# Optimization experiments

Measured on AMD Instinct MI355X. Metric: run time of the kernel, lower is better.

## Reference

```python
import jax, jax.numpy as jnp
import numpy as np

B, F, O = 4096, 16384, 256
MANTISSA_BITS = 23  # flip only mantissa bits to keep values finite


def setup_inputs() -> dict:
    key = jax.random.key(0)
    k1, k2, k3, k4 = jax.random.split(key, 4)
    x = jax.random.normal(k1, (B, F), dtype=jnp.float32)
    W = jax.random.normal(k2, (F, O), dtype=jnp.float32) * 0.02
    b = jnp.zeros((O,), dtype=jnp.float32)
    bitswap_coeff = jnp.ones((), dtype=jnp.float32)  # scalar 'bitswap_coeff' weight
    # uniform categorical over flattened features == uniform randint
    idx = jax.random.randint(k3, (B,), 0, F, dtype=jnp.int32)
    bit_positions = jax.random.randint(k4, (B,), 0, MANTISSA_BITS, dtype=jnp.int32)
    return {"x": x, "W": W, "b": b, "bitswap_coeff": bitswap_coeff,
            "idx": idx, "bit_positions": bit_positions}


def _bit_flip(g, bit_positions):
    # SimulateSwap: flip one mantissa bit of the float32 representation
    gi = jax.lax.bitcast_convert_type(g, jnp.int32)
    gi = gi ^ (jnp.int32(1) << bit_positions)
    return jax.lax.bitcast_convert_type(gi, jnp.float32)


def reference(x, W, b, bitswap_coeff, idx, bit_positions):
    rows = jnp.arange(x.shape[0])
    # gather_nd(batch_dims=1): one element per batch row
    g = x[rows, idx]                              # [B]
    updates = _bit_flip(g, bit_positions) - g     # swap_sim(x) - x
    # tensor_scatter_nd_update onto zeros, scaled by bitswap coefficient
    pert = jnp.zeros_like(x).at[rows, idx].set(updates) * bitswap_coeff
    # wrapped layer: Dense
    return (x + pert) @ W + b
```

## Files before the change

kernel.cpp:

```cpp
#include <hip/hip_runtime.h>

#define M_DIM 4096
#define K_DIM 16384
#define N_DIM 256
#define SPLIT 16

typedef __bf16 bf16x8 __attribute__((ext_vector_type(8)));
typedef __bf16 bf16x4 __attribute__((ext_vector_type(4)));
typedef float f32x4 __attribute__((ext_vector_type(4)));
typedef unsigned short us4 __attribute__((ext_vector_type(4)));

__device__ __forceinline__ unsigned short f2bf(float f) {
  unsigned int u = __float_as_uint(f);
  u += 0x7fffu + ((u >> 16) & 1u);
  return (unsigned short)(u >> 16);
}

__global__ __launch_bounds__(256) void wt_kernel(const float* __restrict__ W,
                                                 __bf16* __restrict__ Wt) {
  __shared__ float tile[64][65];
  const int k0 = blockIdx.x * 64, n0 = blockIdx.y * 64;
  const int t = threadIdx.x;
#pragma unroll
  for (int r = 0; r < 4; ++r) {
    int idx4 = r * 256 + t;
    int kr = idx4 >> 4, c4 = idx4 & 15;
    f32x4 v = *(const f32x4*)(W + (size_t)(k0 + kr) * N_DIM + n0 + c4 * 4);
#pragma unroll
    for (int j = 0; j < 4; ++j) tile[kr][c4 * 4 + j] = v[j];
  }
  __syncthreads();
#pragma unroll
  for (int r = 0; r < 4; ++r) {
    int nr = (t >> 4) + r * 16, k4 = t & 15;
    bf16x4 o;
#pragma unroll
    for (int j = 0; j < 4; ++j) o[j] = (__bf16)tile[k4 * 4 + j][nr];
    *(bf16x4*)(Wt + (size_t)(n0 + nr) * K_DIM + k0 + k4 * 4) = o;
  }
}

__global__ __launch_bounds__(256, 3) void gemm_kernel(const float* __restrict__ x,
                                                      const __bf16* __restrict__ Wt,
                                                      __bf16* __restrict__ part,
                                                      int kslice) {
  __shared__ __bf16 As[64 * 72];
  __shared__ __bf16 Bs[256 * 64];

  const int t = threadIdx.x;
  const int l = t & 63;
  const int w = t >> 6;
  const int la = l & 15, q = l >> 4;
  const int m0 = blockIdx.x * 64;
  const int kbase = blockIdx.y * kslice;

  f32x4 acc[4][4];
  const f32x4 zero = {0.f, 0.f, 0.f, 0.f};
#pragma unroll
  for (int i = 0; i < 4; ++i)
#pragma unroll
    for (int j = 0; j < 4; ++j) acc[i][j] = zero;

  const int niter = kslice >> 6;
  for (int it = 0; it < niter; ++it) {
    const int k0 = kbase + it * 64;

#pragma unroll
    for (int c = 0; c < 8; ++c) {
      int nb = w * 64 + c * 8;
      const __bf16* g = Wt + (size_t)(nb + (l & 7)) * K_DIM + k0 + ((l >> 3) * 8);
      __bf16* lp = &Bs[nb * 64];
      __builtin_amdgcn_global_load_lds((const __attribute__((address_space(1))) void*)g,
                                       (__attribute__((address_space(3))) void*)lp, 16, 0, 0);
    }

#pragma unroll
    for (int r = 0; r < 4; ++r) {
      int idx4 = r * 256 + t;
      int row = idx4 >> 4, c4 = idx4 & 15;
      f32x4 v = *(const f32x4*)(x + (size_t)(m0 + row) * K_DIM + k0 + c4 * 4);
      bf16x4 o = {(__bf16)v[0], (__bf16)v[1], (__bf16)v[2], (__bf16)v[3]};
      *(bf16x4*)(&As[row * 72 + c4 * 4]) = o;
    }
    __syncthreads();

#pragma unroll
    for (int ks = 0; ks < 2; ++ks) {
      const int kb = ks * 32 + q * 8;
      bf16x8 a[4], b[4];
#pragma unroll
      for (int i = 0; i < 4; ++i)
        a[i] = *(const bf16x8*)(&As[(i * 16 + la) * 72 + kb]);
#pragma unroll
      for (int j = 0; j < 4; ++j) {
        int n = w * 64 + j * 16 + la;
        b[j] = *(const bf16x8*)(&Bs[(n >> 3) * 512 + (kb >> 3) * 64 + (n & 7) * 8]);
      }
#pragma unroll
      for (int i = 0; i < 4; ++i)
#pragma unroll
        for (int j = 0; j < 4; ++j)
          acc[i][j] = __builtin_amdgcn_mfma_f32_16x16x32_bf16(a[i], b[j], acc[i][j], 0, 0, 0);
    }
    __syncthreads();
  }

  __bf16* pbase = part + (size_t)blockIdx.y * ((size_t)M_DIM * N_DIM);
#pragma unroll
  for (int i = 0; i < 4; ++i) {
    int r0 = m0 + i * 16 + q * 4;
#pragma unroll
    for (int j = 0; j < 4; ++j) {
      int c = w * 64 + j * 16 + la;
#pragma unroll
      for (int r = 0; r < 4; ++r)
        pbase[(size_t)(r0 + r) * N_DIM + c] = (__bf16)acc[i][j][r];
    }
  }
}

__global__ __launch_bounds__(256) void reduce_kernel(const __bf16* __restrict__ part,
                                                     const float* __restrict__ x,
                                                     const float* __restrict__ W,
                                                     const float* __restrict__ bvec,
                                                     const float* __restrict__ coeffp,
                                                     const int* __restrict__ idx,
                                                     const int* __restrict__ bp,
                                                     float* __restrict__ out) {
  const int row = blockIdx.x;
  const int o = threadIdx.x;
  const int iv = idx[row];
  const float g = x[(size_t)row * K_DIM + iv];
  const int bits = __float_as_int(g) ^ (1 << bp[row]);
  const float upd = __int_as_float(bits) - g;
  const float coeff = coeffp[0];
  const size_t off = (size_t)row * N_DIM + o;
  float sum = 0.f;
#pragma unroll
  for (int s = 0; s < SPLIT; ++s)
    sum += (float)part[(size_t)s * ((size_t)M_DIM * N_DIM) + off];
  out[off] = sum + coeff * upd * W[(size_t)iv * N_DIM + o] + bvec[o];
}

extern "C" void kernel_launch(void* const* d_in, const int* in_sizes, int n_in,
                              void* d_out, int out_size, void* d_ws, size_t ws_size,
                              hipStream_t stream) {
  const float* x = (const float*)d_in[0];
  const float* W = (const float*)d_in[1];
  const float* b = (const float*)d_in[2];
  const float* coeff = (const float*)d_in[3];
  const int* idx = (const int*)d_in[4];
  const int* bp = (const int*)d_in[5];
  float* out = (float*)d_out;

  __bf16* Wt = (__bf16*)d_ws;
  const size_t wt_bytes = (size_t)K_DIM * N_DIM * 2;
  __bf16* part = (__bf16*)((char*)d_ws + wt_bytes);

  hipLaunchKernelGGL(wt_kernel, dim3(K_DIM / 64, N_DIM / 64), dim3(256), 0, stream, W, Wt);
  hipLaunchKernelGGL(gemm_kernel, dim3(M_DIM / 64, SPLIT), dim3(256), 0, stream,
                     x, Wt, part, K_DIM / SPLIT);
  hipLaunchKernelGGL(reduce_kernel, dim3(M_DIM), dim3(256), 0, stream,
                     part, x, W, b, coeff, idx, bp, out);
}
```

Before: 435.4 us.

## Register-prefetch next K tile in GEMM, pad B smem layout, halve split-K

Replaces the direct global-to-LDS loads for the B operand with register staging, and prefetches the next iteration's A and B tiles into registers while the MFMAs run on the current tile. B shared memory becomes a padded row-major layout, and split-K drops from 16 to 8, which halves partial-sum traffic and the reduce work. The costs are higher register pressure under the 3-blocks-per-CU launch bound and half as many blocks in the GEMM grid.

```diff
diff --git a/kernel.cpp b/kernel.cpp
--- a/kernel.cpp
+++ b/kernel.cpp
@@ -3,18 +3,14 @@
 #define M_DIM 4096
 #define K_DIM 16384
 #define N_DIM 256
-#define SPLIT 16
+#define SPLIT 8
+#define BK 64
+#define KSLICE (K_DIM / SPLIT)
+#define NITER (KSLICE / BK)
 
 typedef __bf16 bf16x8 __attribute__((ext_vector_type(8)));
 typedef __bf16 bf16x4 __attribute__((ext_vector_type(4)));
 typedef float f32x4 __attribute__((ext_vector_type(4)));
-typedef unsigned short us4 __attribute__((ext_vector_type(4)));
-
-__device__ __forceinline__ unsigned short f2bf(float f) {
-  unsigned int u = __float_as_uint(f);
-  u += 0x7fffu + ((u >> 16) & 1u);
-  return (unsigned short)(u >> 16);
-}
 
 __global__ __launch_bounds__(256) void wt_kernel(const float* __restrict__ W,
                                                  __bf16* __restrict__ Wt) {
@@ -42,17 +38,30 @@
 
 __global__ __launch_bounds__(256, 3) void gemm_kernel(const float* __restrict__ x,
                                                       const __bf16* __restrict__ Wt,
-                                                      __bf16* __restrict__ part,
-                                                      int kslice) {
+                                                      __bf16* __restrict__ part) {
   __shared__ __bf16 As[64 * 72];
-  __shared__ __bf16 Bs[256 * 64];
+  __shared__ __bf16 Bs[256 * 72];
 
   const int t = threadIdx.x;
   const int l = t & 63;
   const int w = t >> 6;
   const int la = l & 15, q = l >> 4;
   const int m0 = blockIdx.x * 64;
-  const int kbase = blockIdx.y * kslice;
+  const int kbase = blockIdx.y * KSLICE;
+
+  const int arow = t >> 4, ac4 = t & 15;
+  const int bn = t >> 3, bk8 = (t & 7) * 8;
+
+  const float* ap = x + (size_t)(m0 + arow) * K_DIM + kbase + ac4 * 4;
+  const __bf16* bp = Wt + (size_t)bn * K_DIM + kbase + bk8;
+
+  f32x4 areg[4];
+  bf16x8 breg[8];
+
+#pragma unroll
+  for (int r = 0; r < 4; ++r) areg[r] = *(const f32x4*)(ap + (size_t)r * 16 * K_DIM);
+#pragma unroll
+  for (int c = 0; c < 8; ++c) breg[c] = *(const bf16x8*)(bp + (size_t)c * 32 * K_DIM);
 
   f32x4 acc[4][4];
   const f32x4 zero = {0.f, 0.f, 0.f, 0.f};
@@ -61,28 +70,27 @@
 #pragma unroll
     for (int j = 0; j < 4; ++j) acc[i][j] = zero;
 
-  const int niter = kslice >> 6;
-  for (int it = 0; it < niter; ++it) {
-    const int k0 = kbase + it * 64;
-
-#pragma unroll
-    for (int c = 0; c < 8; ++c) {
-      int nb = w * 64 + c * 8;
-      const __bf16* g = Wt + (size_t)(nb + (l & 7)) * K_DIM + k0 + ((l >> 3) * 8);
-      __bf16* lp = &Bs[nb * 64];
-      __builtin_amdgcn_global_load_lds((const __attribute__((address_space(1))) void*)g,
-                                       (__attribute__((address_space(3))) void*)lp, 16, 0, 0);
-    }
-
+  for (int it = 0; it < NITER; ++it) {
+    __syncthreads();
 #pragma unroll
     for (int r = 0; r < 4; ++r) {
-      int idx4 = r * 256 + t;
-      int row = idx4 >> 4, c4 = idx4 & 15;
-      f32x4 v = *(const f32x4*)(x + (size_t)(m0 + row) * K_DIM + k0 + c4 * 4);
-      bf16x4 o = {(__bf16)v[0], (__bf16)v[1], (__bf16)v[2], (__bf16)v[3]};
-      *(bf16x4*)(&As[row * 72 + c4 * 4]) = o;
+      bf16x4 o = {(__bf16)areg[r][0], (__bf16)areg[r][1],
+                  (__bf16)areg[r][2], (__bf16)areg[r][3]};
+      *(bf16x4*)(&As[(arow + r * 16) * 72 + ac4 * 4]) = o;
     }
+#pragma unroll
+    for (int c = 0; c < 8; ++c)
+      *(bf16x8*)(&Bs[(bn + c * 32) * 72 + bk8]) = breg[c];
     __syncthreads();
+
+    if (it + 1 < NITER) {
+      ap += BK;
+      bp += BK;
+#pragma unroll
+      for (int r = 0; r < 4; ++r) areg[r] = *(const f32x4*)(ap + (size_t)r * 16 * K_DIM);
+#pragma unroll
+      for (int c = 0; c < 8; ++c) breg[c] = *(const bf16x8*)(bp + (size_t)c * 32 * K_DIM);
+    }
 
 #pragma unroll
     for (int ks = 0; ks < 2; ++ks) {
@@ -92,17 +100,14 @@
       for (int i = 0; i < 4; ++i)
         a[i] = *(const bf16x8*)(&As[(i * 16 + la) * 72 + kb]);
 #pragma unroll
-      for (int j = 0; j < 4; ++j) {
-        int n = w * 64 + j * 16 + la;
-        b[j] = *(const bf16x8*)(&Bs[(n >> 3) * 512 + (kb >> 3) * 64 + (n & 7) * 8]);
-      }
+      for (int j = 0; j < 4; ++j)
+        b[j] = *(const bf16x8*)(&Bs[(w * 64 + j * 16 + la) * 72 + kb]);
 #pragma unroll
       for (int i = 0; i < 4; ++i)
 #pragma unroll
         for (int j = 0; j < 4; ++j)
           acc[i][j] = __builtin_amdgcn_mfma_f32_16x16x32_bf16(a[i], b[j], acc[i][j], 0, 0, 0);
     }
-    __syncthreads();
   }
 
   __bf16* pbase = part + (size_t)blockIdx.y * ((size_t)M_DIM * N_DIM);
@@ -159,7 +164,7 @@
 
   hipLaunchKernelGGL(wt_kernel, dim3(K_DIM / 64, N_DIM / 64), dim3(256), 0, stream, W, Wt);
   hipLaunchKernelGGL(gemm_kernel, dim3(M_DIM / 64, SPLIT), dim3(256), 0, stream,
-                     x, Wt, part, K_DIM / SPLIT);
+                     x, Wt, part);
   hipLaunchKernelGGL(reduce_kernel, dim3(M_DIM), dim3(256), 0, stream,
                      part, x, W, b, coeff, idx, bp, out);
 }
```

New measurement: 413.7 us. -5.0%, faster.
